# Performance work log

Hardware: AMD Instinct MI355X
Metric: run time of the kernel (lower is better)

Reference implementation:

```python
import jax, jax.numpy as jnp
import numpy as np

B = 64          # graphs per batch
N_PER = 1024    # nodes per graph
N = B * N_PER   # 65536 total nodes
E_PER = 8192    # edges per graph (sorted by graph)
E = B * E_PER   # 524288 total edges
HID = 256       # config.model.dim_hidden
RATIO = 0.5     # causal_ratio
N_RES = int(RATIO * E_PER)  # edges kept per graph (n_reserve)


def setup_inputs() -> dict:
    key = jax.random.key(0)
    ks = jax.random.split(key, 12)
    x = jax.random.normal(ks[0], (N, HID), jnp.float32)
    # per-graph edges, no self-loops, sorted by graph id (split_batch assumption)
    base = jnp.repeat(jnp.arange(B, dtype=jnp.int32) * N_PER, E_PER)
    row_loc = jax.random.randint(ks[1], (E,), 0, N_PER, dtype=jnp.int32)
    off = jax.random.randint(ks[2], (E,), 1, N_PER, dtype=jnp.int32)
    col_loc = (row_loc + off) % N_PER
    edge_index = jnp.stack([base + row_loc, base + col_loc])  # [2, E]
    batch = jnp.repeat(jnp.arange(B, dtype=jnp.int32), N_PER)  # [N]

    def lin(k, fan_in, shape):
        return (jax.random.normal(k, shape, jnp.float32) / np.sqrt(fan_in)).astype(jnp.float32)

    # 2-layer GIN MLP params (eps = 0)
    W11 = lin(ks[3], HID, (HID, HID)); b11 = jnp.zeros((HID,), jnp.float32)
    W12 = lin(ks[4], HID, (HID, HID)); b12 = jnp.zeros((HID,), jnp.float32)
    W21 = lin(ks[5], HID, (HID, HID)); b21 = jnp.zeros((HID,), jnp.float32)
    W22 = lin(ks[6], HID, (HID, HID)); b22 = jnp.zeros((HID,), jnp.float32)
    # edge scoring linear: Linear(2*HID, 1)
    w_score = lin(ks[7], 2 * HID, (2 * HID,))
    b_score = jnp.zeros((), jnp.float32)
    return {"x": x, "edge_index": edge_index, "batch": batch,
            "W11": W11, "b11": b11, "W12": W12, "b12": b12,
            "W21": W21, "b21": b21, "W22": W22, "b22": b22,
            "w_score": w_score, "b_score": b_score}


def _gin_layer(h, row, col, W1, b1, W2, b2):
    agg = jax.ops.segment_sum(h[col], row, num_segments=N)  # sum over in-edges
    h = h + agg  # (1 + eps) * x + aggregate, eps = 0
    h = jax.nn.relu(h @ W1 + b1)
    return jax.nn.relu(h @ W2 + b2)


def _relabel(h, batch, ei_sub):
    # torch: sub_nodes = unique(edge_index); compact + remap. Padded to N for fixed shapes.
    sub = jnp.unique(ei_sub, size=N, fill_value=N)  # [N], padded with sentinel N
    node_idx = jnp.zeros((N + 1,), jnp.int32).at[sub].set(jnp.arange(N, dtype=jnp.int32))
    h_pad = jnp.concatenate([h, jnp.zeros((1, h.shape[1]), h.dtype)], axis=0)
    b_pad = jnp.concatenate([batch, jnp.full((1,), -1, batch.dtype)], axis=0)
    return h_pad[sub], node_idx[ei_sub], b_pad[sub]


def reference(x, edge_index, batch, W11, b11, W12, b12, W21, b21, W22, b22, w_score, b_score):
    row, col = edge_index[0], edge_index[1]
    h = _gin_layer(x, row, col, W11, b11, W12, b12)
    h = _gin_layer(h, row, col, W21, b21, W22, b22)  # [N, HID]

    # edge_score = Linear(cat(h[row], h[col])) without materializing [E, 2*HID]
    s_src = h @ w_score[:HID]   # [N]
    s_dst = h @ w_score[HID:]   # [N]
    edge_score = s_src[row] + s_dst[col] + b_score  # [E]

    # per-graph sort-based top-k split (split_graph), batched over B graphs
    s = edge_score.reshape(B, E_PER)
    rank = jnp.argsort(-s, axis=1)                      # descending
    idx_res, idx_drop = rank[:, :N_RES], rank[:, N_RES:]
    ei = edge_index.reshape(2, B, E_PER)

    def gather_edges(idx):
        return jnp.take_along_axis(ei, jnp.broadcast_to(idx[None], (2, B, idx.shape[1])), axis=2).reshape(2, -1)

    causal_ei = gather_edges(idx_res)
    conf_ei = gather_edges(idx_drop)
    causal_w = jnp.take_along_axis(s, idx_res, axis=1).reshape(-1)
    conf_w = -jnp.take_along_axis(s, idx_drop, axis=1).reshape(-1)

    causal_x, causal_ei_rel, causal_batch = _relabel(h, batch, causal_ei)
    conf_x, conf_ei_rel, conf_batch = _relabel(h, batch, conf_ei)

    return (causal_x, causal_ei_rel, causal_w, causal_batch,
            conf_x, conf_ei_rel, conf_w, conf_batch, edge_score)
```

## Files before the change

### kernel.cpp

```cpp
#include <hip/hip_runtime.h>
#include <hip/hip_bf16.h>

#define NN      65536
#define EE      524288
#define HIDC    256
#define BB      64
#define EPB     8192
#define NPB     1024
#define NRES    4096

#define O_CX    0
#define O_CEI   16777216
#define O_CW    17301504
#define O_CB    17563648
#define O_FX    17629184
#define O_FEI   34406400
#define O_FW    34930688
#define O_FB    35192832
#define O_ES    35258368

typedef __attribute__((ext_vector_type(8))) short short8v;
typedef __attribute__((ext_vector_type(4))) float f32x4;

__device__ __forceinline__ unsigned f2ord(float f) {
    unsigned u = __float_as_uint(f);
    return (u & 0x80000000u) ? ~u : (u | 0x80000000u);
}
__device__ __forceinline__ float ord2f(unsigned m) {
    unsigned u = (m & 0x80000000u) ? (m & 0x7FFFFFFFu) : ~m;
    return __uint_as_float(u);
}

__device__ __forceinline__ unsigned packsplit(float v) {
    unsigned u = __float_as_uint(v);
    unsigned hi = (u + 0x7FFFu + ((u >> 16) & 1u)) & 0xFFFF0000u;
    float lo = v - __uint_as_float(hi);
    unsigned ul = __float_as_uint(lo);
    unsigned lo16 = (ul + 0x7FFFu + ((ul >> 16) & 1u)) >> 16;
    return hi | lo16;
}

__global__ void k_init(int* __restrict__ flagC, int* __restrict__ flagF,
                       float* __restrict__ sSrc, float* __restrict__ sDst) {
    int v = blockIdx.x * blockDim.x + threadIdx.x;
    if (v < NN) { flagC[v] = 0; flagF[v] = 0; sSrc[v] = 0.f; sDst[v] = 0.f; }
}

__global__ void k_wsplit(const float* __restrict__ W11, const float* __restrict__ W12,
                         const float* __restrict__ W21, const float* __restrict__ W22,
                         unsigned* __restrict__ Wtp) {
    int g = blockIdx.x * 256 + threadIdx.x;
    int w = g >> 16, r = g & 65535;
    int n = r >> 8, k = r & 255;
    const float* W = (w == 0) ? W11 : (w == 1) ? W12 : (w == 2) ? W21 : W22;
    Wtp[g] = packsplit(W[k * 256 + n]);
}

__global__ __launch_bounds__(1024) void k_csr(const int* __restrict__ row,
                                              const int* __restrict__ col,
                                              int* __restrict__ rowPtr,
                                              int* __restrict__ colSorted) {
    __shared__ int hist[NPB];
    __shared__ int scn[NPB];
    int b = blockIdx.x, t = threadIdx.x;
    int base = b * EPB;
    hist[t] = 0;
    __syncthreads();
    int r[8], c[8];
#pragma unroll
    for (int j = 0; j < 8; ++j) {
        int e = base + t + j * 1024;
        r[j] = row[e] & (NPB - 1);
        c[j] = col[e];
        atomicAdd(&hist[r[j]], 1);
    }
    __syncthreads();
    int v = hist[t];
    scn[t] = v;
    __syncthreads();
    for (int off = 1; off < 1024; off <<= 1) {
        int a = (t >= off) ? scn[t - off] : 0;
        __syncthreads();
        scn[t] += a;
        __syncthreads();
    }
    int start = scn[t] - v;
    rowPtr[b * NPB + t] = base + start;
    if (b == 0 && t == 0) rowPtr[NN] = EE;
    hist[t] = start;
    __syncthreads();
#pragma unroll
    for (int j = 0; j < 8; ++j) {
        int pos = atomicAdd(&hist[r[j]], 1);
        colSorted[base + pos] = c[j];
    }
}

__global__ __launch_bounds__(512) void k_agg_lds(const float* __restrict__ src,
                                                 const int* __restrict__ colSorted,
                                                 const int* __restrict__ rowPtr,
                                                 unsigned* __restrict__ dstP) {
    __shared__ float lds[NPB * 16];
    int ch = blockIdx.x, b = blockIdx.y;
    int t = threadIdx.x;
    int nbase = b * NPB;
    const float4* sp = (const float4*)src;
    float4* lp4 = (float4*)lds;
#pragma unroll
    for (int p = 0; p < 8; ++p) {
        int i = t + p * 512;
        int node = i >> 2, f4 = i & 3;
        lp4[node * 4 + f4] = sp[(size_t)(nbase + node) * 64 + ch * 4 + f4];
    }
    __syncthreads();
    const float2* lds2 = (const float2*)lds;
    int g = t >> 3, l = t & 7;
    int v0 = nbase + g * 16;
    for (int i = 0; i < 16; ++i) {
        int v = v0 + i;
        int e0 = rowPtr[v], e1 = rowPtr[v + 1];
        float2 acc = lds2[(v - nbase) * 8 + l];
        for (int e = e0; e < e1; ++e) {
            int c = colSorted[e] & (NPB - 1);
            float2 s = lds2[c * 8 + l];
            acc.x += s.x; acc.y += s.y;
        }
        uint2 o = make_uint2(packsplit(acc.x), packsplit(acc.y));
        *((uint2*)dstP + (size_t)v * 128 + ch * 8 + l) = o;
    }
}

template<int EPI, int SC>
__global__ __launch_bounds__(256) void k_gemm_mfma(const unsigned* __restrict__ Ap,
                                                   const unsigned* __restrict__ Wtp,
                                                   const float* __restrict__ bias,
                                                   void* __restrict__ Cout,
                                                   const float* __restrict__ wsc,
                                                   float* __restrict__ sSrc,
                                                   float* __restrict__ sDst) {
    __shared__ short Ah[128][40];
    __shared__ short Al[128][40];
    __shared__ short Bh[128][40];
    __shared__ short Bl[128][40];
    int t = threadIdx.x;
    int lane = t & 63, wave = t >> 6;
    int bm = blockIdx.x * 128, bn = blockIdx.y * 128;
    int ln = lane & 15, qd = lane >> 4;
    f32x4 acc[2][8];
#pragma unroll
    for (int i = 0; i < 2; ++i)
#pragma unroll
        for (int j = 0; j < 8; ++j) acc[i][j] = (f32x4){0.f, 0.f, 0.f, 0.f};
    int row = t >> 1, half = t & 1;
    const uint4* ag = (const uint4*)(Ap + (size_t)(bm + row) * 256) + half * 4;
    const uint4* bg = (const uint4*)(Wtp + (size_t)(bn + row) * 256) + half * 4;
    for (int k0 = 0; k0 < 256; k0 += 32) {
        uint4 av[4], bv[4];
#pragma unroll
        for (int s = 0; s < 4; ++s) { av[s] = ag[s]; bv[s] = bg[s]; }
        ag += 8; bg += 8;
        __syncthreads();
#pragma unroll
        for (int s = 0; s < 4; ++s) {
            int kc = half * 16 + s * 4;
            *(short4*)&Ah[row][kc] = make_short4((short)(av[s].x >> 16), (short)(av[s].y >> 16),
                                                 (short)(av[s].z >> 16), (short)(av[s].w >> 16));
            *(short4*)&Al[row][kc] = make_short4((short)av[s].x, (short)av[s].y,
                                                 (short)av[s].z, (short)av[s].w);
            *(short4*)&Bh[row][kc] = make_short4((short)(bv[s].x >> 16), (short)(bv[s].y >> 16),
                                                 (short)(bv[s].z >> 16), (short)(bv[s].w >> 16));
            *(short4*)&Bl[row][kc] = make_short4((short)bv[s].x, (short)bv[s].y,
                                                 (short)bv[s].z, (short)bv[s].w);
        }
        __syncthreads();
        short8v ah0 = *(short8v*)&Ah[wave * 32 + ln][qd * 8];
        short8v ah1 = *(short8v*)&Ah[wave * 32 + 16 + ln][qd * 8];
        short8v al0 = *(short8v*)&Al[wave * 32 + ln][qd * 8];
        short8v al1 = *(short8v*)&Al[wave * 32 + 16 + ln][qd * 8];
#pragma unroll
        for (int nt = 0; nt < 8; ++nt) {
            short8v bh = *(short8v*)&Bh[nt * 16 + ln][qd * 8];
            short8v bl = *(short8v*)&Bl[nt * 16 + ln][qd * 8];
            f32x4 c0 = acc[0][nt];
            c0 = __builtin_amdgcn_mfma_f32_16x16x32_bf16(al0, bh, c0, 0, 0, 0);
            c0 = __builtin_amdgcn_mfma_f32_16x16x32_bf16(ah0, bl, c0, 0, 0, 0);
            c0 = __builtin_amdgcn_mfma_f32_16x16x32_bf16(ah0, bh, c0, 0, 0, 0);
            acc[0][nt] = c0;
            f32x4 c1 = acc[1][nt];
            c1 = __builtin_amdgcn_mfma_f32_16x16x32_bf16(al1, bh, c1, 0, 0, 0);
            c1 = __builtin_amdgcn_mfma_f32_16x16x32_bf16(ah1, bl, c1, 0, 0, 0);
            c1 = __builtin_amdgcn_mfma_f32_16x16x32_bf16(ah1, bh, c1, 0, 0, 0);
            acc[1][nt] = c1;
        }
    }
    float ps[2][4] = {}, pd[2][4] = {};
#pragma unroll
    for (int nt = 0; nt < 8; ++nt) {
        float bvs = bias[bn + nt * 16 + ln];
        float ws = 0.f, wd = 0.f;
        if (SC) { ws = wsc[bn + nt * 16 + ln]; wd = wsc[256 + bn + nt * 16 + ln]; }
#pragma unroll
        for (int mt = 0; mt < 2; ++mt)
#pragma unroll
            for (int r = 0; r < 4; ++r) {
                int gm = bm + wave * 32 + mt * 16 + qd * 4 + r;
                int gn = bn + nt * 16 + ln;
                float v = acc[mt][nt][r] + bvs;
                v = v > 0.f ? v : 0.f;
                if (SC) { ps[mt][r] += v * ws; pd[mt][r] += v * wd; }
                if (EPI == 0) ((unsigned*)Cout)[(size_t)gm * 256 + gn] = packsplit(v);
                else          ((float*)Cout)[(size_t)gm * 256 + gn] = v;
            }
    }
    if (SC) {
#pragma unroll
        for (int off = 1; off < 16; off <<= 1)
#pragma unroll
            for (int mt = 0; mt < 2; ++mt)
#pragma unroll
                for (int r = 0; r < 4; ++r) {
                    ps[mt][r] += __shfl_xor(ps[mt][r], off, 64);
                    pd[mt][r] += __shfl_xor(pd[mt][r], off, 64);
                }
        if (ln == 0) {
#pragma unroll
            for (int mt = 0; mt < 2; ++mt)
#pragma unroll
                for (int r = 0; r < 4; ++r) {
                    int gm = bm + wave * 32 + mt * 16 + qd * 4 + r;
                    atomicAdd(&sSrc[gm], ps[mt][r]);
                    atomicAdd(&sDst[gm], pd[mt][r]);
                }
        }
    }
}

__global__ __launch_bounds__(512) void k_sortS1(const int* __restrict__ row, const int* __restrict__ col,
                                                const float* __restrict__ sSrc, const float* __restrict__ sDst,
                                                const float* __restrict__ bsc,
                                                float* __restrict__ esc,
                                                unsigned long long* __restrict__ keys) {
    __shared__ unsigned long long lds[4096];
    int blk = blockIdx.x, b = blk >> 1, c = blk & 1;
    int t = threadIdx.x;
    int gbase = b * EPB + c * 4096;
    float bb = bsc[0];
    for (int i = t; i < 4096; i += 512) {
        int idx = c * 4096 + i;
        int ge = b * EPB + idx;
        float s = sSrc[row[ge]] + sDst[col[ge]] + bb;
        esc[ge] = s;
        unsigned m = f2ord(s);
        lds[i] = ((unsigned long long)(~m) << 32) | (unsigned)idx;
    }
    __syncthreads();
    bool dirbit = (c != 0);
    for (int k = 2; k <= 4096; k <<= 1) {
        for (int j = k >> 1; j > 0; j >>= 1) {
            for (int t2 = t; t2 < 2048; t2 += 512) {
                int i = ((t2 & ~(j - 1)) << 1) | (t2 & (j - 1));
                int l = i | j;
                unsigned long long a = lds[i], d = lds[l];
                bool up = (((i & k) == 0) != dirbit);
                if ((a > d) == up) { lds[i] = d; lds[l] = a; }
            }
            __syncthreads();
        }
    }
    for (int i = t; i < 4096; i += 512) keys[gbase + i] = lds[i];
}

__global__ void k_sortS2(unsigned long long* __restrict__ keys) {
    int g = blockIdx.x * 256 + threadIdx.x;
    int b = g >> 12, i = g & 4095;
    unsigned long long* p = keys + b * EPB;
    unsigned long long a = p[i], d = p[i + 4096];
    if (a > d) { p[i] = d; p[i + 4096] = a; }
}

__global__ __launch_bounds__(512) void k_sortS3(const unsigned long long* __restrict__ keys,
                                                const int* __restrict__ row, const int* __restrict__ col,
                                                int* __restrict__ perm,
                                                int* __restrict__ flagC, int* __restrict__ flagF,
                                                float* __restrict__ outCW, float* __restrict__ outFW) {
    __shared__ unsigned long long lds[4096];
    int blk = blockIdx.x, b = blk >> 1, c = blk & 1;
    int gbase = b * EPB + c * 4096;
    int t = threadIdx.x;
    for (int i = t; i < 4096; i += 512) lds[i] = keys[gbase + i];
    __syncthreads();
    for (int j = 2048; j > 0; j >>= 1) {
        for (int t2 = t; t2 < 2048; t2 += 512) {
            int i = ((t2 & ~(j - 1)) << 1) | (t2 & (j - 1));
            int l = i | j;
            unsigned long long a = lds[i], d = lds[l];
            if (a > d) { lds[i] = d; lds[l] = a; }
        }
        __syncthreads();
    }
    for (int i = t; i < 4096; i += 512) {
        unsigned long long kk = lds[i];
        int idx = (int)(kk & 0x1FFFull);
        int ge = b * EPB + idx;
        perm[gbase + i] = idx;
        int r = row[ge], cl = col[ge];
        float s = ord2f(~(unsigned)(kk >> 32));
        if (c == 0) { flagC[r] = 1; flagC[cl] = 1; outCW[b * NRES + i] = s; }
        else        { flagF[r] = 1; flagF[cl] = 1; outFW[b * NRES + i] = -s; }
    }
}

__global__ __launch_bounds__(256) void k_scan1(const int* __restrict__ fc, const int* __restrict__ ff,
                                               int* __restrict__ bsC, int* __restrict__ bsF) {
    __shared__ int s1[256], s2[256];
    int t = threadIdx.x, v = blockIdx.x * 256 + t;
    s1[t] = fc[v]; s2[t] = ff[v];
    __syncthreads();
    for (int off = 128; off > 0; off >>= 1) {
        if (t < off) { s1[t] += s1[t + off]; s2[t] += s2[t + off]; }
        __syncthreads();
    }
    if (t == 0) { bsC[blockIdx.x] = s1[0]; bsF[blockIdx.x] = s2[0]; }
}

__global__ __launch_bounds__(256) void k_scan2(const int* __restrict__ bsC, const int* __restrict__ bsF,
                                               int* __restrict__ boC, int* __restrict__ boF,
                                               int* __restrict__ prefC, int* __restrict__ prefF) {
    __shared__ int s1[256], s2[256];
    int t = threadIdx.x;
    int v1 = bsC[t], v2 = bsF[t];
    s1[t] = v1; s2[t] = v2;
    __syncthreads();
    for (int off = 1; off < 256; off <<= 1) {
        int a1 = (t >= off) ? s1[t - off] : 0;
        int a2 = (t >= off) ? s2[t - off] : 0;
        __syncthreads();
        s1[t] += a1; s2[t] += a2;
        __syncthreads();
    }
    boC[t] = s1[t] - v1; boF[t] = s2[t] - v2;
    if (t == 255) { prefC[NN] = s1[255]; prefF[NN] = s2[255]; }
}

__global__ __launch_bounds__(256) void k_scan3(const int* __restrict__ fc, const int* __restrict__ ff,
                                               const int* __restrict__ boC, const int* __restrict__ boF,
                                               int* __restrict__ prefC, int* __restrict__ prefF) {
    __shared__ int s1[256], s2[256];
    int t = threadIdx.x, v = blockIdx.x * 256 + t;
    int f1 = fc[v], f2 = ff[v];
    s1[t] = f1; s2[t] = f2;
    __syncthreads();
    for (int off = 1; off < 256; off <<= 1) {
        int a1 = (t >= off) ? s1[t - off] : 0;
        int a2 = (t >= off) ? s2[t - off] : 0;
        __syncthreads();
        s1[t] += a1; s2[t] += a2;
        __syncthreads();
    }
    prefC[v] = boC[blockIdx.x] + s1[t] - f1;
    prefF[v] = boF[blockIdx.x] + s2[t] - f2;
}

__global__ __launch_bounds__(256) void k_scatter2(const int* __restrict__ flagC, const int* __restrict__ prefC,
                                                  const int* __restrict__ flagF, const int* __restrict__ prefF,
                                                  const float* __restrict__ h,
                                                  float* __restrict__ outCX, float* __restrict__ outCB,
                                                  float* __restrict__ outFX, float* __restrict__ outFB) {
    int lane = threadIdx.x & 63;
    int i = blockIdx.x * 4 + (threadIdx.x >> 6);
    int c0 = lane << 2;
    int fC = flagC[i], fF = flagF[i];
    float4 hv = make_float4(0.f, 0.f, 0.f, 0.f);
    if (fC | fF) hv = *(const float4*)(h + (size_t)i * HIDC + c0);
    if (fC) {
        int p = prefC[i];
        *(float4*)(outCX + (size_t)p * HIDC + c0) = hv;
        if (lane == 0) outCB[p] = (float)(i >> 10);
    }
    if (fF) {
        int p = prefF[i];
        *(float4*)(outFX + (size_t)p * HIDC + c0) = hv;
        if (lane == 0) outFB[p] = (float)(i >> 10);
    }
    int nuC = prefC[NN], nuF = prefF[NN];
    float4 z = make_float4(0.f, 0.f, 0.f, 0.f);
    if (i >= nuC) { *(float4*)(outCX + (size_t)i * HIDC + c0) = z; if (lane == 0) outCB[i] = -1.0f; }
    if (i >= nuF) { *(float4*)(outFX + (size_t)i * HIDC + c0) = z; if (lane == 0) outFB[i] = -1.0f; }
}

__global__ void k_eirel(const int* __restrict__ perm, const int* __restrict__ row,
                        const int* __restrict__ col, const int* __restrict__ prefC,
                        const int* __restrict__ prefF,
                        float* __restrict__ outC, float* __restrict__ outF) {
    int g = blockIdx.x * blockDim.x + threadIdx.x;
    if (g >= EE) return;
    int b = g >> 13, jj = g & (EPB - 1);
    int ge = (b << 13) | perm[g];
    int r = row[ge], c = col[ge];
    if (jj < NRES) {
        int idx = b * NRES + jj;
        outC[idx] = (float)prefC[r];
        outC[BB * NRES + idx] = (float)prefC[c];
    } else {
        int idx = b * NRES + (jj - NRES);
        outF[idx] = (float)prefF[r];
        outF[BB * NRES + idx] = (float)prefF[c];
    }
}

extern "C" void kernel_launch(void* const* d_in, const int* in_sizes, int n_in,
                              void* d_out, int out_size, void* d_ws, size_t ws_size,
                              hipStream_t stream) {
    const float* x   = (const float*)d_in[0];
    const int*   ei  = (const int*)d_in[1];
    const int*   row = ei;
    const int*   col = ei + EE;
    const float* W11 = (const float*)d_in[3];
    const float* b11 = (const float*)d_in[4];
    const float* W12 = (const float*)d_in[5];
    const float* b12 = (const float*)d_in[6];
    const float* W21 = (const float*)d_in[7];
    const float* b21 = (const float*)d_in[8];
    const float* W22 = (const float*)d_in[9];
    const float* b22 = (const float*)d_in[10];
    const float* wsc = (const float*)d_in[11];
    const float* bsc = (const float*)d_in[12];

    float* out = (float*)d_out;

    void* X = (void*)(out + O_CX);

    char* w = (char*)d_ws;
    auto alloc = [&](size_t bytes) { char* p = w; w += (bytes + 255) & ~(size_t)255; return p; };
    void*  P         = (void*)alloc((size_t)NN * HIDC * 4);
    float* sSrc      = (float*)alloc((size_t)NN * 4);
    float* sDst      = (float*)alloc((size_t)NN * 4);
    int*   colSorted = (int*)alloc((size_t)EE * 4);
    int*   rowPtr    = (int*)alloc((size_t)(NN + 1) * 4);
    int*   perm      = (int*)alloc((size_t)EE * 4);
    unsigned long long* keys64 = (unsigned long long*)alloc((size_t)EE * 8);
    int*   flagC     = (int*)alloc((size_t)NN * 4);
    int*   flagF     = (int*)alloc((size_t)NN * 4);
    int*   prefC     = (int*)alloc((size_t)(NN + 1) * 4);
    int*   prefF     = (int*)alloc((size_t)(NN + 1) * 4);
    unsigned* Wtp    = (unsigned*)alloc((size_t)4 * 65536 * 4);
    int*   bsC       = (int*)alloc(256 * 4);
    int*   bsF       = (int*)alloc(256 * 4);
    int*   boC       = (int*)alloc(256 * 4);
    int*   boF       = (int*)alloc(256 * 4);

    float* esc = out + O_ES;

    hipLaunchKernelGGL(k_init, dim3(NN / 256), dim3(256), 0, stream, flagC, flagF, sSrc, sDst);
    hipLaunchKernelGGL(k_wsplit, dim3(1024), dim3(256), 0, stream, W11, W12, W21, W22, Wtp);
    hipLaunchKernelGGL(k_csr, dim3(BB), dim3(1024), 0, stream, row, col, rowPtr, colSorted);

    dim3 ggrid(NN / 128, 2), gblk(256);
    dim3 agrid(16, BB), ablk(512);

    hipLaunchKernelGGL(k_agg_lds, agrid, ablk, 0, stream, x, colSorted, rowPtr, (unsigned*)X);
    k_gemm_mfma<0, 0><<<ggrid, gblk, 0, stream>>>((const unsigned*)X, Wtp + 0 * 65536, b11, P,
                                                  nullptr, nullptr, nullptr);
    k_gemm_mfma<1, 0><<<ggrid, gblk, 0, stream>>>((const unsigned*)P, Wtp + 1 * 65536, b12, X,
                                                  nullptr, nullptr, nullptr);
    hipLaunchKernelGGL(k_agg_lds, agrid, ablk, 0, stream, (const float*)X, colSorted, rowPtr,
                       (unsigned*)P);
    k_gemm_mfma<0, 0><<<ggrid, gblk, 0, stream>>>((const unsigned*)P, Wtp + 2 * 65536, b21, X,
                                                  nullptr, nullptr, nullptr);
    k_gemm_mfma<1, 1><<<ggrid, gblk, 0, stream>>>((const unsigned*)X, Wtp + 3 * 65536, b22, P,
                                                  wsc, sSrc, sDst);

    const float* h = (const float*)P;

    hipLaunchKernelGGL(k_sortS1, dim3(BB * 2), dim3(512), 0, stream, row, col, sSrc, sDst, bsc,
                       esc, keys64);
    hipLaunchKernelGGL(k_sortS2, dim3(EE / 512), dim3(256), 0, stream, keys64);
    hipLaunchKernelGGL(k_sortS3, dim3(BB * 2), dim3(512), 0, stream, keys64, row, col,
                       perm, flagC, flagF, out + O_CW, out + O_FW);

    hipLaunchKernelGGL(k_scan1, dim3(NN / 256), dim3(256), 0, stream, flagC, flagF, bsC, bsF);
    hipLaunchKernelGGL(k_scan2, dim3(1), dim3(256), 0, stream, bsC, bsF, boC, boF, prefC, prefF);
    hipLaunchKernelGGL(k_scan3, dim3(NN / 256), dim3(256), 0, stream, flagC, flagF, boC, boF, prefC, prefF);

    hipLaunchKernelGGL(k_scatter2, dim3(NN / 4), dim3(256), 0, stream, flagC, prefC, flagF, prefF, h,
                       out + O_CX, out + O_CB, out + O_FX, out + O_FB);
    hipLaunchKernelGGL(k_eirel, dim3(EE / 256), dim3(256), 0, stream, perm, row, col,
                       prefC, prefF, out + O_CEI, out + O_FEI);
}
```

Baseline: 706.7 us.

## Replace row-per-thread CSR aggregation with edge-parallel LDS atomic aggregation

The CSR builder now emits packed (row,col) edges sorted by row instead of rowPtr plus colSorted. The new aggregation kernel gives each thread 16 consecutive sorted edges and sums runs of equal row in registers. Each run is flushed with LDS float atomics into an accumulator tile, processing 8-feature chunks, four per block. This removes the load imbalance of the degree-variable per-node loops and the per-node rowPtr reads, at the cost of LDS atomics and extra syncs per chunk.

```diff
diff --git a/kernel.cpp b/kernel.cpp
--- a/kernel.cpp
+++ b/kernel.cpp
@@ -58,8 +58,7 @@
 
 __global__ __launch_bounds__(1024) void k_csr(const int* __restrict__ row,
                                               const int* __restrict__ col,
-                                              int* __restrict__ rowPtr,
-                                              int* __restrict__ colSorted) {
+                                              unsigned* __restrict__ edgePacked) {
     __shared__ int hist[NPB];
     __shared__ int scn[NPB];
     int b = blockIdx.x, t = threadIdx.x;
@@ -71,7 +70,7 @@
     for (int j = 0; j < 8; ++j) {
         int e = base + t + j * 1024;
         r[j] = row[e] & (NPB - 1);
-        c[j] = col[e];
+        c[j] = col[e] & (NPB - 1);
         atomicAdd(&hist[r[j]], 1);
     }
     __syncthreads();
@@ -85,48 +84,70 @@
         __syncthreads();
     }
     int start = scn[t] - v;
-    rowPtr[b * NPB + t] = base + start;
-    if (b == 0 && t == 0) rowPtr[NN] = EE;
     hist[t] = start;
     __syncthreads();
 #pragma unroll
     for (int j = 0; j < 8; ++j) {
         int pos = atomicAdd(&hist[r[j]], 1);
-        colSorted[base + pos] = c[j];
-    }
-}
-
-__global__ __launch_bounds__(512) void k_agg_lds(const float* __restrict__ src,
-                                                 const int* __restrict__ colSorted,
-                                                 const int* __restrict__ rowPtr,
-                                                 unsigned* __restrict__ dstP) {
-    __shared__ float lds[NPB * 16];
-    int ch = blockIdx.x, b = blockIdx.y;
-    int t = threadIdx.x;
+        edgePacked[base + pos] = ((unsigned)r[j] << 10) | (unsigned)c[j];
+    }
+}
+
+__global__ __launch_bounds__(512) void k_agg_e(const float* __restrict__ src,
+                                               const unsigned* __restrict__ edgePacked,
+                                               unsigned* __restrict__ dstP) {
+    __shared__ float srcS[NPB * 8];
+    __shared__ float accS[NPB * 8];
+    int cg = blockIdx.x, b = blockIdx.y, t = threadIdx.x;
     int nbase = b * NPB;
+    const uint4* ep = (const uint4*)(edgePacked + (size_t)b * EPB) + t * 4;
+    uint4 e0 = ep[0], e1 = ep[1], e2 = ep[2], e3 = ep[3];
+    unsigned earr[16] = {e0.x, e0.y, e0.z, e0.w, e1.x, e1.y, e1.z, e1.w,
+                         e2.x, e2.y, e2.z, e2.w, e3.x, e3.y, e3.z, e3.w};
     const float4* sp = (const float4*)src;
-    float4* lp4 = (float4*)lds;
-#pragma unroll
-    for (int p = 0; p < 8; ++p) {
-        int i = t + p * 512;
-        int node = i >> 2, f4 = i & 3;
-        lp4[node * 4 + f4] = sp[(size_t)(nbase + node) * 64 + ch * 4 + f4];
-    }
-    __syncthreads();
-    const float2* lds2 = (const float2*)lds;
-    int g = t >> 3, l = t & 7;
-    int v0 = nbase + g * 16;
-    for (int i = 0; i < 16; ++i) {
-        int v = v0 + i;
-        int e0 = rowPtr[v], e1 = rowPtr[v + 1];
-        float2 acc = lds2[(v - nbase) * 8 + l];
-        for (int e = e0; e < e1; ++e) {
-            int c = colSorted[e] & (NPB - 1);
-            float2 s = lds2[c * 8 + l];
-            acc.x += s.x; acc.y += s.y;
-        }
-        uint2 o = make_uint2(packsplit(acc.x), packsplit(acc.y));
-        *((uint2*)dstP + (size_t)v * 128 + ch * 8 + l) = o;
+    float4* s4 = (float4*)srcS;
+    float4* a4 = (float4*)accS;
+    for (int cc = 0; cc < 4; ++cc) {
+        int ch = cg * 4 + cc;
+#pragma unroll
+        for (int p = 0; p < 4; ++p) {
+            int i = t + p * 512;
+            float4 v = sp[(size_t)(nbase + (i >> 1)) * 64 + ch * 2 + (i & 1)];
+            s4[i] = v; a4[i] = v;
+        }
+        __syncthreads();
+        float a[8] = {0.f, 0.f, 0.f, 0.f, 0.f, 0.f, 0.f, 0.f};
+        int curRow = -1;
+#pragma unroll
+        for (int j = 0; j < 16; ++j) {
+            unsigned e = earr[j];
+            int r = (int)(e >> 10), c = (int)(e & 1023u);
+            if (r != curRow) {
+                if (curRow >= 0) {
+#pragma unroll
+                    for (int i = 0; i < 8; ++i) atomicAdd(&accS[curRow * 8 + i], a[i]);
+                }
+#pragma unroll
+                for (int i = 0; i < 8; ++i) a[i] = 0.f;
+                curRow = r;
+            }
+            float4 v0 = s4[c * 2], v1 = s4[c * 2 + 1];
+            a[0] += v0.x; a[1] += v0.y; a[2] += v0.z; a[3] += v0.w;
+            a[4] += v1.x; a[5] += v1.y; a[6] += v1.z; a[7] += v1.w;
+        }
+        if (curRow >= 0) {
+#pragma unroll
+            for (int i = 0; i < 8; ++i) atomicAdd(&accS[curRow * 8 + i], a[i]);
+        }
+        __syncthreads();
+#pragma unroll
+        for (int p = 0; p < 4; ++p) {
+            int i = t + p * 512;
+            float4 v = a4[i];
+            uint4 o = make_uint4(packsplit(v.x), packsplit(v.y), packsplit(v.z), packsplit(v.w));
+            *((uint4*)dstP + (size_t)(nbase + (i >> 1)) * 64 + ch * 2 + (i & 1)) = o;
+        }
+        __syncthreads();
     }
 }
 
@@ -435,8 +456,7 @@
     void*  P         = (void*)alloc((size_t)NN * HIDC * 4);
     float* sSrc      = (float*)alloc((size_t)NN * 4);
     float* sDst      = (float*)alloc((size_t)NN * 4);
-    int*   colSorted = (int*)alloc((size_t)EE * 4);
-    int*   rowPtr    = (int*)alloc((size_t)(NN + 1) * 4);
+    unsigned* edgePacked = (unsigned*)alloc((size_t)EE * 4);
     int*   perm      = (int*)alloc((size_t)EE * 4);
     unsigned long long* keys64 = (unsigned long long*)alloc((size_t)EE * 8);
     int*   flagC     = (int*)alloc((size_t)NN * 4);
@@ -453,18 +473,17 @@
 
     hipLaunchKernelGGL(k_init, dim3(NN / 256), dim3(256), 0, stream, flagC, flagF, sSrc, sDst);
     hipLaunchKernelGGL(k_wsplit, dim3(1024), dim3(256), 0, stream, W11, W12, W21, W22, Wtp);
-    hipLaunchKernelGGL(k_csr, dim3(BB), dim3(1024), 0, stream, row, col, rowPtr, colSorted);
+    hipLaunchKernelGGL(k_csr, dim3(BB), dim3(1024), 0, stream, row, col, edgePacked);
 
     dim3 ggrid(NN / 128, 2), gblk(256);
-    dim3 agrid(16, BB), ablk(512);
-
-    hipLaunchKernelGGL(k_agg_lds, agrid, ablk, 0, stream, x, colSorted, rowPtr, (unsigned*)X);
+    dim3 agrid(8, BB), ablk(512);
+
+    hipLaunchKernelGGL(k_agg_e, agrid, ablk, 0, stream, x, edgePacked, (unsigned*)X);
     k_gemm_mfma<0, 0><<<ggrid, gblk, 0, stream>>>((const unsigned*)X, Wtp + 0 * 65536, b11, P,
                                                   nullptr, nullptr, nullptr);
     k_gemm_mfma<1, 0><<<ggrid, gblk, 0, stream>>>((const unsigned*)P, Wtp + 1 * 65536, b12, X,
                                                   nullptr, nullptr, nullptr);
-    hipLaunchKernelGGL(k_agg_lds, agrid, ablk, 0, stream, (const float*)X, colSorted, rowPtr,
-                       (unsigned*)P);
+    hipLaunchKernelGGL(k_agg_e, agrid, ablk, 0, stream, (const float*)X, edgePacked, (unsigned*)P);
     k_gemm_mfma<0, 0><<<ggrid, gblk, 0, stream>>>((const unsigned*)P, Wtp + 2 * 65536, b21, X,
                                                   nullptr, nullptr, nullptr);
     k_gemm_mfma<1, 1><<<ggrid, gblk, 0, stream>>>((const unsigned*)X, Wtp + 3 * 65536, b22, P,
```

Result: slower. 814.0 us (+15.2%).
